# Performance work log

Hardware: AMD Instinct MI355X
Metric: run time of the kernel (lower is better)

The kernel has to match this reference:

```python
import jax, jax.numpy as jnp
import numpy as np

B, T, C, H, RANK = 4, 2048, 1024, 16, 8


def _lora_linear(x, W, b, A, Bm):
    # loralib-style: y = x W^T + b + (x A^T) B^T  (scaling alpha/r = 1)
    return x @ W.T + b + (x @ A.T) @ Bm.T


def setup_inputs() -> dict:
    key = jax.random.key(0)
    ks = jax.random.split(key, 6)
    s_in = 1.0 / np.sqrt(C)
    return {
        "x": jax.random.normal(ks[0], (B, T, C), jnp.float32),
        "c_attn_w": jax.random.normal(ks[1], (3 * C, C), jnp.float32) * s_in,
        "c_attn_b": jnp.zeros((3 * C,), jnp.float32),
        "c_attn_A": jax.random.normal(ks[2], (RANK, C), jnp.float32) * s_in,
        "c_attn_B": jnp.zeros((3 * C, RANK), jnp.float32),
        "c_proj_w": jax.random.normal(ks[3], (C, C), jnp.float32) * s_in,
        "c_proj_b": jnp.zeros((C,), jnp.float32),
        "c_proj_A": jax.random.normal(ks[4], (RANK, C), jnp.float32) * s_in,
        "c_proj_B": jnp.zeros((C, RANK), jnp.float32),
        "n_head": H,
    }


def reference(x, c_attn_w, c_attn_b, c_attn_A, c_attn_B,
              c_proj_w, c_proj_b, c_proj_A, c_proj_B, n_head):
    Bsz, Tlen, Cd = x.shape
    d = Cd // n_head
    qkv = _lora_linear(x, c_attn_w, c_attn_b, c_attn_A, c_attn_B)  # [B,T,3C]
    q, k, v = jnp.split(qkv, 3, axis=2)
    query, key_out = q, k  # returned pre-reshape, as in torch
    # [B, H, T, d]
    qh = q.reshape(Bsz, Tlen, n_head, d).transpose(0, 2, 1, 3)
    kh = k.reshape(Bsz, Tlen, n_head, d).transpose(0, 2, 1, 3)
    vh = v.reshape(Bsz, Tlen, n_head, d).transpose(0, 2, 1, 3)
    att = jnp.einsum('bhqd,bhkd->bhqk', qh, kh) * (1.0 / np.sqrt(d))
    causal = jnp.tril(jnp.ones((Tlen, Tlen), bool))
    att = jnp.where(causal[None, None], att, -jnp.inf)
    att = jax.nn.softmax(att, axis=-1)
    y = jnp.einsum('bhqk,bhkd->bhqd', att, vh)
    y = y.transpose(0, 2, 1, 3).reshape(Bsz, Tlen, Cd)
    out = _lora_linear(y, c_proj_w, c_proj_b, c_proj_A, c_proj_B)
    return out, query, key_out
```

## Files before the change

### kernel.cpp

```cpp
#include <hip/hip_runtime.h>
#include <stdint.h>

#define T_LEN 2048
#define C_DIM 1024
#define NHEAD 16
#define DHEAD 64
#define QOFF  8388608L
#define KOFF  16777216L
#define SCALE_LOG2 0.18033688011112042f

typedef float f32x4 __attribute__((ext_vector_type(4)));
typedef short bf16x8 __attribute__((ext_vector_type(8)));
typedef short s16x4 __attribute__((ext_vector_type(4)));
typedef unsigned short u16;

__device__ __forceinline__ float b2f(u16 h) {
  union { uint32_t u; float f; } v; v.u = ((uint32_t)h) << 16; return v.f;
}
__device__ __forceinline__ u16 f2b(float f) {
  union { float f; uint32_t u; } v; v.f = f;
  uint32_t r = v.u + 0x7fffu + ((v.u >> 16) & 1u);
  return (u16)(r >> 16);
}
__device__ __forceinline__ u16 f2b_tr(float f) {
  union { float f; uint32_t u; } v; v.f = f;
  return (u16)(v.u >> 16);
}
__device__ __forceinline__ void async16(const u16* g, u16* l) {
  __builtin_amdgcn_global_load_lds((const __attribute__((address_space(1))) void*)g,
                                   (__attribute__((address_space(3))) void*)l, 16, 0, 0);
}

#define MFMA16 __builtin_amdgcn_mfma_f32_16x16x32_bf16

__global__ __launch_bounds__(256) void prep_all(const float* __restrict__ x,
                                                u16* __restrict__ xc,
                                                const float* __restrict__ w1,
                                                const float* __restrict__ B1,
                                                const float* __restrict__ A1,
                                                u16* __restrict__ w1e,
                                                const float* __restrict__ w2,
                                                const float* __restrict__ B2,
                                                const float* __restrict__ A2,
                                                u16* __restrict__ w2e) {
  int b = blockIdx.x;
  if (b < 8192) {
    long i = ((long)b * 256 + threadIdx.x) * 4;
    f32x4 v = *(const f32x4*)(x + i);
    s16x4 r;
    r[0] = (short)f2b(v[0]); r[1] = (short)f2b(v[1]);
    r[2] = (short)f2b(v[2]); r[3] = (short)f2b(v[3]);
    *(s16x4*)(xc + i) = r;
  } else if (b < 20480) {
    int i = (b - 8192) * 256 + threadIdx.x;
    int n = i >> 10, k = i & 1023;
    float acc = w1[i];
#pragma unroll
    for (int r = 0; r < 8; r++) acc += B1[n * 8 + r] * A1[r * 1024 + k];
    w1e[i] = f2b(acc);
  } else {
    int i = (b - 20480) * 256 + threadIdx.x;
    int n = i >> 10, k = i & 1023;
    float acc = w2[i];
#pragma unroll
    for (int r = 0; r < 8; r++) acc += B2[n * 8 + r] * A2[r * 1024 + k];
    w2e[i] = f2b(acc);
  }
}

template <int MODE>
__global__ __launch_bounds__(256) void gemm_bt(const u16* __restrict__ A,
                                               const u16* __restrict__ Bt,
                                               const float* __restrict__ bias,
                                               float* __restrict__ outf,
                                               u16* __restrict__ kc,
                                               u16* __restrict__ vblk, int K) {
  __shared__ __align__(16) u16 ldsA[128 * 32];
  __shared__ __align__(16) u16 ldsB[128 * 32];
  const int t = threadIdx.x;
  const int lane = t & 63, l15 = lane & 15, quad = lane >> 4, w = t >> 6;
  const int wr = (w >> 1) * 64, wc = (w & 1) * 64;
  const long rowA = (long)blockIdx.y * 128;
  const long rowB = (long)blockIdx.x * 128;
  const int srow = t >> 2, scol = (t & 3) * 8;

  f32x4 acc[4][4];
#pragma unroll
  for (int i = 0; i < 4; i++)
#pragma unroll
    for (int j = 0; j < 4; j++) { f32x4 z = {0.f, 0.f, 0.f, 0.f}; acc[i][j] = z; }

  const u16* Ab = A + rowA * K;
  const u16* Bb = Bt + rowB * K;
  for (int k0 = 0; k0 < K; k0 += 32) {
    __syncthreads();
    async16(Ab + (long)srow * K + k0 + scol, &ldsA[t * 8]);
    async16(Ab + (long)(srow + 64) * K + k0 + scol, &ldsA[2048 + t * 8]);
    async16(Bb + (long)srow * K + k0 + scol, &ldsB[t * 8]);
    async16(Bb + (long)(srow + 64) * K + k0 + scol, &ldsB[2048 + t * 8]);
    __syncthreads();
    bf16x8 af[4], bfr[4];
#pragma unroll
    for (int g = 0; g < 4; g++) {
      af[g]  = *(const bf16x8*)&ldsA[(wr + g * 16 + l15) * 32 + quad * 8];
      bfr[g] = *(const bf16x8*)&ldsB[(wc + g * 16 + l15) * 32 + quad * 8];
    }
#pragma unroll
    for (int i = 0; i < 4; i++)
#pragma unroll
      for (int j = 0; j < 4; j++)
        acc[i][j] = MFMA16(af[i], bfr[j], acc[i][j], 0, 0, 0);
  }

#pragma unroll
  for (int i = 0; i < 4; i++) {
#pragma unroll
    for (int j = 0; j < 4; j++) {
      int n = (int)rowB + wc + j * 16 + l15;
      float bv = bias[n];
#pragma unroll
      for (int r = 0; r < 4; r++) {
        int m = (int)rowA + wr + i * 16 + quad * 4 + r;
        float val = acc[i][j][r] + bv;
        if constexpr (MODE == 1) {
          outf[(long)m * C_DIM + n] = val;
        } else {
          int sec = n >> 10;
          int nc = n & 1023;
          int h = nc >> 6, dd = nc & 63;
          int bb = m >> 11, tt = m & 2047;
          int bh = bb * NHEAD + h;
          if (sec == 0) {
            outf[QOFF + (long)m * C_DIM + nc] = val;
          } else if (sec == 1) {
            outf[KOFF + (long)m * C_DIM + nc] = val;
            kc[(long)bh * (T_LEN * 64) + (long)tt * 64 + dd] = f2b(val);
          } else {
            vblk[(long)bh * (T_LEN * 64) + (long)(tt >> 6) * 4096 + dd * 64 + (tt & 63)] = f2b(val);
          }
        }
      }
    }
  }
}

__global__ __launch_bounds__(256) void flash_attn(const float* __restrict__ qsec,
                                                  const u16* __restrict__ kc,
                                                  const u16* __restrict__ vblk,
                                                  u16* __restrict__ yb) {
  __shared__ __align__(16) u16 ldsK[2][64 * 64];
  __shared__ __align__(16) u16 ldsV[2][64 * 64];
  __shared__ __align__(16) u16 plds[4][32 * 72];
  const int t = threadIdx.x;
  const int lane = t & 63, l15 = lane & 15, quad = lane >> 4, w = t >> 6;
  const int p = blockIdx.x >> 6;
  const int bh = blockIdx.x & 63;
  const int bb = bh >> 4, h = bh & 15;

  bf16x8 ones;
#pragma unroll
  for (int j = 0; j < 8; j++) ones[j] = (short)0x3F80;

  const u16* kcb = kc + (long)bh * (T_LEN * 64);
  const u16* vbb = vblk + (long)bh * (T_LEN * 64);
  const int l0 = t, l1 = 256 + t;
  const int s0c = ((l0 >> 3) * 8 + ((l0 & 7) ^ ((l0 >> 3) & 7))) * 8;
  const int s1c = ((l1 >> 3) * 8 + ((l1 & 7) ^ ((l1 >> 3) & 7))) * 8;

#define KV_STAGE(kt_, b_) do {                                        \
    const u16* ks_ = kcb + (long)(kt_) * 4096;                        \
    const u16* vs_ = vbb + (long)(kt_) * 4096;                        \
    async16(ks_ + s0c, &ldsK[b_][l0 * 8]);                            \
    async16(ks_ + s1c, &ldsK[b_][l1 * 8]);                            \
    async16(vs_ + s0c, &ldsV[b_][l0 * 8]);                            \
    async16(vs_ + s1c, &ldsV[b_][l1 * 8]);                            \
  } while (0)

#pragma unroll 1
  for (int half = 0; half < 2; half++) {
    const int qt = half ? p : (15 - p);
    const int q0 = qt * 128;

    const float* Qb = qsec + ((long)bb * T_LEN + q0 + w * 32) * C_DIM + h * DHEAD;
    bf16x8 qf[2][2];
#pragma unroll
    for (int rg = 0; rg < 2; rg++)
#pragma unroll
      for (int kk = 0; kk < 2; kk++) {
        const float* ptr = Qb + (long)(rg * 16 + l15) * C_DIM + kk * 32 + quad * 8;
        f32x4 a = *(const f32x4*)ptr, b = *(const f32x4*)(ptr + 4);
        bf16x8 r;
        r[0] = (short)f2b(a[0] * SCALE_LOG2); r[1] = (short)f2b(a[1] * SCALE_LOG2);
        r[2] = (short)f2b(a[2] * SCALE_LOG2); r[3] = (short)f2b(a[3] * SCALE_LOG2);
        r[4] = (short)f2b(b[0] * SCALE_LOG2); r[5] = (short)f2b(b[1] * SCALE_LOG2);
        r[6] = (short)f2b(b[2] * SCALE_LOG2); r[7] = (short)f2b(b[3] * SCALE_LOG2);
        qf[rg][kk] = r;
      }

    f32x4 o[2][4];
    f32x4 ls[2];
#pragma unroll
    for (int rg = 0; rg < 2; rg++) {
#pragma unroll
      for (int cg = 0; cg < 4; cg++) { f32x4 z = {0.f, 0.f, 0.f, 0.f}; o[rg][cg] = z; }
      f32x4 z = {0.f, 0.f, 0.f, 0.f}; ls[rg] = z;
    }

    const int qminw = q0 + w * 32;
    const int nkt = (q0 + 128) >> 6;

    KV_STAGE(0, 0);
    asm volatile("s_waitcnt vmcnt(0)" ::: "memory");
    __builtin_amdgcn_s_barrier();

    for (int kt = 0; kt < nkt; kt++) {
      const int kb0 = kt * 64;
      const int cur = kt & 1;
      if (kt + 1 < nkt) KV_STAGE(kt + 1, cur ^ 1);

      if (kb0 <= qminw + 31) {
        f32x4 s[2][4];
#pragma unroll
        for (int rg = 0; rg < 2; rg++)
#pragma unroll
          for (int kg = 0; kg < 4; kg++) { f32x4 z = {0.f, 0.f, 0.f, 0.f}; s[rg][kg] = z; }
#pragma unroll
        for (int kg = 0; kg < 4; kg++) {
          int row = kg * 16 + l15, sw = row & 7;
          bf16x8 kf0 = *(const bf16x8*)&ldsK[cur][row * 64 + ((quad ^ sw) * 8)];
          bf16x8 kf1 = *(const bf16x8*)&ldsK[cur][row * 64 + (((4 + quad) ^ sw) * 8)];
#pragma unroll
          for (int rg = 0; rg < 2; rg++) {
            s[rg][kg] = MFMA16(qf[rg][0], kf0, s[rg][kg], 0, 0, 0);
            s[rg][kg] = MFMA16(qf[rg][1], kf1, s[rg][kg], 0, 0, 0);
          }
        }
        const bool needMask = (kb0 + 63) > qminw;
#pragma unroll
        for (int rg = 0; rg < 2; rg++) {
#pragma unroll
          for (int r = 0; r < 4; r++) {
            float v0 = s[rg][0][r], v1 = s[rg][1][r], v2 = s[rg][2][r], v3 = s[rg][3][r];
            if (needMask) {
              int qrow = qminw + rg * 16 + quad * 4 + r;
              if (kb0 + l15 > qrow)      v0 = -3.0e38f;
              if (kb0 + 16 + l15 > qrow) v1 = -3.0e38f;
              if (kb0 + 32 + l15 > qrow) v2 = -3.0e38f;
              if (kb0 + 48 + l15 > qrow) v3 = -3.0e38f;
            }
            int prow = rg * 16 + quad * 4 + r;
            plds[w][prow * 72 + l15]      = f2b_tr(exp2f(v0));
            plds[w][prow * 72 + 16 + l15] = f2b_tr(exp2f(v1));
            plds[w][prow * 72 + 32 + l15] = f2b_tr(exp2f(v2));
            plds[w][prow * 72 + 48 + l15] = f2b_tr(exp2f(v3));
          }
        }
        asm volatile("s_waitcnt lgkmcnt(0)" ::: "memory");
        bf16x8 pf[2][2];
#pragma unroll
        for (int rg = 0; rg < 2; rg++)
#pragma unroll
          for (int kk = 0; kk < 2; kk++)
            pf[rg][kk] = *(const bf16x8*)&plds[w][(rg * 16 + l15) * 72 + kk * 32 + quad * 8];
#pragma unroll
        for (int rg = 0; rg < 2; rg++) {
          ls[rg] = MFMA16(pf[rg][0], ones, ls[rg], 0, 0, 0);
          ls[rg] = MFMA16(pf[rg][1], ones, ls[rg], 0, 0, 0);
        }
#pragma unroll
        for (int cg = 0; cg < 4; cg++) {
          int row = cg * 16 + l15, sw = row & 7;
          bf16x8 vf0 = *(const bf16x8*)&ldsV[cur][row * 64 + ((quad ^ sw) * 8)];
          bf16x8 vf1 = *(const bf16x8*)&ldsV[cur][row * 64 + (((4 + quad) ^ sw) * 8)];
#pragma unroll
          for (int rg = 0; rg < 2; rg++) {
            o[rg][cg] = MFMA16(pf[rg][0], vf0, o[rg][cg], 0, 0, 0);
            o[rg][cg] = MFMA16(pf[rg][1], vf1, o[rg][cg], 0, 0, 0);
          }
        }
      }

      asm volatile("s_waitcnt vmcnt(0)" ::: "memory");
      __builtin_amdgcn_s_barrier();
    }

#pragma unroll
    for (int rg = 0; rg < 2; rg++) {
#pragma unroll
      for (int r = 0; r < 4; r++) {
        float inv = 1.0f / ls[rg][r];
        int tt = q0 + w * 32 + rg * 16 + quad * 4 + r;
        long base = ((long)bb * T_LEN + tt) * C_DIM + h * DHEAD;
#pragma unroll
        for (int cg = 0; cg < 4; cg++)
          yb[base + cg * 16 + l15] = f2b(o[rg][cg][r] * inv);
      }
    }
  }
}

extern "C" void kernel_launch(void* const* d_in, const int* in_sizes, int n_in,
                              void* d_out, int out_size, void* d_ws, size_t ws_size,
                              hipStream_t stream) {
  const float* x  = (const float*)d_in[0];
  const float* w1 = (const float*)d_in[1];
  const float* b1 = (const float*)d_in[2];
  const float* A1 = (const float*)d_in[3];
  const float* B1 = (const float*)d_in[4];
  const float* w2 = (const float*)d_in[5];
  const float* b2 = (const float*)d_in[6];
  const float* A2 = (const float*)d_in[7];
  const float* B2 = (const float*)d_in[8];
  float* outf = (float*)d_out;
  u16* outb16 = (u16*)d_out;

  u16* ws  = (u16*)d_ws;
  u16* w2e = ws;
  u16* w1e = ws + 1048576;
  u16* xc  = ws + 4194304;
  u16* yb  = ws + 1048576;
  u16* vblk = outb16;
  u16* kcp  = outb16 + 8388608;

  prep_all<<<24576, 256, 0, stream>>>(x, xc, w1, B1, A1, w1e, w2, B2, A2, w2e);
  gemm_bt<0><<<dim3(24, 64), 256, 0, stream>>>(xc, w1e, b1, outf, kcp, vblk, 1024);
  flash_attn<<<512, 256, 0, stream>>>(outf + QOFF, kcp, vblk, yb);
  gemm_bt<1><<<dim3(8, 64), 256, 0, stream>>>(yb, w2e, b2, outf, nullptr, nullptr, 1024);
}
```

Before: 355.8 us.

## Load K/V fragments directly from global memory and drop LDS staging

The flash attention kernel no longer stages K and V tiles into double-buffered shared memory with async copies and block barriers. Each wave now reads its K and V MFMA fragments straight from global memory and runs its own causal trip count. The launch also changes from 512 blocks that each processed a paired short and long query tile to 1024 blocks of one query tile each. This removes barrier sync and LDS footprint, which may allow higher occupancy. The cost is redundant global/L2 reads across the four waves, no explicit prefetch to hide load latency, and loss of the paired-tile load balancing.

Result: slower. 413.4 us (+16.2%).

```diff
diff --git a/kernel.cpp b/kernel.cpp
--- a/kernel.cpp
+++ b/kernel.cpp
@@ -148,153 +148,128 @@
                                                   const u16* __restrict__ kc,
                                                   const u16* __restrict__ vblk,
                                                   u16* __restrict__ yb) {
-  __shared__ __align__(16) u16 ldsK[2][64 * 64];
-  __shared__ __align__(16) u16 ldsV[2][64 * 64];
   __shared__ __align__(16) u16 plds[4][32 * 72];
   const int t = threadIdx.x;
   const int lane = t & 63, l15 = lane & 15, quad = lane >> 4, w = t >> 6;
-  const int p = blockIdx.x >> 6;
+  const int qt = 15 - (blockIdx.x >> 6);
   const int bh = blockIdx.x & 63;
+  const int q0 = qt * 128;
   const int bb = bh >> 4, h = bh & 15;
 
+  const float* Qb = qsec + ((long)bb * T_LEN + q0 + w * 32) * C_DIM + h * DHEAD;
+  bf16x8 qf[2][2];
+#pragma unroll
+  for (int rg = 0; rg < 2; rg++)
+#pragma unroll
+    for (int kk = 0; kk < 2; kk++) {
+      const float* p = Qb + (long)(rg * 16 + l15) * C_DIM + kk * 32 + quad * 8;
+      f32x4 a = *(const f32x4*)p, b = *(const f32x4*)(p + 4);
+      bf16x8 r;
+      r[0] = (short)f2b(a[0] * SCALE_LOG2); r[1] = (short)f2b(a[1] * SCALE_LOG2);
+      r[2] = (short)f2b(a[2] * SCALE_LOG2); r[3] = (short)f2b(a[3] * SCALE_LOG2);
+      r[4] = (short)f2b(b[0] * SCALE_LOG2); r[5] = (short)f2b(b[1] * SCALE_LOG2);
+      r[6] = (short)f2b(b[2] * SCALE_LOG2); r[7] = (short)f2b(b[3] * SCALE_LOG2);
+      qf[rg][kk] = r;
+    }
+
   bf16x8 ones;
 #pragma unroll
   for (int j = 0; j < 8; j++) ones[j] = (short)0x3F80;
+
+  f32x4 o[2][4];
+  f32x4 ls[2];
+#pragma unroll
+  for (int rg = 0; rg < 2; rg++) {
+#pragma unroll
+    for (int cg = 0; cg < 4; cg++) { f32x4 z = {0.f, 0.f, 0.f, 0.f}; o[rg][cg] = z; }
+    f32x4 z = {0.f, 0.f, 0.f, 0.f}; ls[rg] = z;
+  }
 
   const u16* kcb = kc + (long)bh * (T_LEN * 64);
   const u16* vbb = vblk + (long)bh * (T_LEN * 64);
-  const int l0 = t, l1 = 256 + t;
-  const int s0c = ((l0 >> 3) * 8 + ((l0 & 7) ^ ((l0 >> 3) & 7))) * 8;
-  const int s1c = ((l1 >> 3) * 8 + ((l1 & 7) ^ ((l1 >> 3) & 7))) * 8;
-
-#define KV_STAGE(kt_, b_) do {                                        \
-    const u16* ks_ = kcb + (long)(kt_) * 4096;                        \
-    const u16* vs_ = vbb + (long)(kt_) * 4096;                        \
-    async16(ks_ + s0c, &ldsK[b_][l0 * 8]);                            \
-    async16(ks_ + s1c, &ldsK[b_][l1 * 8]);                            \
-    async16(vs_ + s0c, &ldsV[b_][l0 * 8]);                            \
-    async16(vs_ + s1c, &ldsV[b_][l1 * 8]);                            \
-  } while (0)
-
-#pragma unroll 1
-  for (int half = 0; half < 2; half++) {
-    const int qt = half ? p : (15 - p);
-    const int q0 = qt * 128;
-
-    const float* Qb = qsec + ((long)bb * T_LEN + q0 + w * 32) * C_DIM + h * DHEAD;
-    bf16x8 qf[2][2];
+
+  const int qminw = q0 + w * 32;
+  const int nktw = (qminw + 95) >> 6;
+
+  for (int kt = 0; kt < nktw; kt++) {
+    const int kb0 = kt * 64;
+    const u16* ktb = kcb + (long)kb0 * 64;
+    const u16* vtb = vbb + (long)kt * 4096;
+
+    f32x4 s[2][4];
 #pragma unroll
     for (int rg = 0; rg < 2; rg++)
 #pragma unroll
-      for (int kk = 0; kk < 2; kk++) {
-        const float* ptr = Qb + (long)(rg * 16 + l15) * C_DIM + kk * 32 + quad * 8;
-        f32x4 a = *(const f32x4*)ptr, b = *(const f32x4*)(ptr + 4);
-        bf16x8 r;
-        r[0] = (short)f2b(a[0] * SCALE_LOG2); r[1] = (short)f2b(a[1] * SCALE_LOG2);
-        r[2] = (short)f2b(a[2] * SCALE_LOG2); r[3] = (short)f2b(a[3] * SCALE_LOG2);
-        r[4] = (short)f2b(b[0] * SCALE_LOG2); r[5] = (short)f2b(b[1] * SCALE_LOG2);
-        r[6] = (short)f2b(b[2] * SCALE_LOG2); r[7] = (short)f2b(b[3] * SCALE_LOG2);
-        qf[rg][kk] = r;
+      for (int kg = 0; kg < 4; kg++) { f32x4 z = {0.f, 0.f, 0.f, 0.f}; s[rg][kg] = z; }
+#pragma unroll
+    for (int kg = 0; kg < 4; kg++) {
+      int row = kg * 16 + l15;
+      bf16x8 kf0 = *(const bf16x8*)(ktb + row * 64 + quad * 8);
+      bf16x8 kf1 = *(const bf16x8*)(ktb + row * 64 + 32 + quad * 8);
+#pragma unroll
+      for (int rg = 0; rg < 2; rg++) {
+        s[rg][kg] = MFMA16(qf[rg][0], kf0, s[rg][kg], 0, 0, 0);
+        s[rg][kg] = MFMA16(qf[rg][1], kf1, s[rg][kg], 0, 0, 0);
       }
-
-    f32x4 o[2][4];
-    f32x4 ls[2];
+    }
+    const bool needMask = (kb0 + 63) > qminw;
 #pragma unroll
     for (int rg = 0; rg < 2; rg++) {
 #pragma unroll
-      for (int cg = 0; cg < 4; cg++) { f32x4 z = {0.f, 0.f, 0.f, 0.f}; o[rg][cg] = z; }
-      f32x4 z = {0.f, 0.f, 0.f, 0.f}; ls[rg] = z;
-    }
-
-    const int qminw = q0 + w * 32;
-    const int nkt = (q0 + 128) >> 6;
-
-    KV_STAGE(0, 0);
-    asm volatile("s_waitcnt vmcnt(0)" ::: "memory");
-    __builtin_amdgcn_s_barrier();
-
-    for (int kt = 0; kt < nkt; kt++) {
-      const int kb0 = kt * 64;
-      const int cur = kt & 1;
-      if (kt + 1 < nkt) KV_STAGE(kt + 1, cur ^ 1);
-
-      if (kb0 <= qminw + 31) {
-        f32x4 s[2][4];
-#pragma unroll
-        for (int rg = 0; rg < 2; rg++)
-#pragma unroll
-          for (int kg = 0; kg < 4; kg++) { f32x4 z = {0.f, 0.f, 0.f, 0.f}; s[rg][kg] = z; }
-#pragma unroll
-        for (int kg = 0; kg < 4; kg++) {
-          int row = kg * 16 + l15, sw = row & 7;
-          bf16x8 kf0 = *(const bf16x8*)&ldsK[cur][row * 64 + ((quad ^ sw) * 8)];
-          bf16x8 kf1 = *(const bf16x8*)&ldsK[cur][row * 64 + (((4 + quad) ^ sw) * 8)];
-#pragma unroll
-          for (int rg = 0; rg < 2; rg++) {
-            s[rg][kg] = MFMA16(qf[rg][0], kf0, s[rg][kg], 0, 0, 0);
-            s[rg][kg] = MFMA16(qf[rg][1], kf1, s[rg][kg], 0, 0, 0);
-          }
+      for (int r = 0; r < 4; r++) {
+        float v0 = s[rg][0][r], v1 = s[rg][1][r], v2 = s[rg][2][r], v3 = s[rg][3][r];
+        if (needMask) {
+          int qrow = qminw + rg * 16 + quad * 4 + r;
+          if (kb0 + l15 > qrow)      v0 = -3.0e38f;
+          if (kb0 + 16 + l15 > qrow) v1 = -3.0e38f;
+          if (kb0 + 32 + l15 > qrow) v2 = -3.0e38f;
+          if (kb0 + 48 + l15 > qrow) v3 = -3.0e38f;
         }
-        const bool needMask = (kb0 + 63) > qminw;
-#pragma unroll
-        for (int rg = 0; rg < 2; rg++) {
-#pragma unroll
-          for (int r = 0; r < 4; r++) {
-            float v0 = s[rg][0][r], v1 = s[rg][1][r], v2 = s[rg][2][r], v3 = s[rg][3][r];
-            if (needMask) {
-              int qrow = qminw + rg * 16 + quad * 4 + r;
-              if (kb0 + l15 > qrow)      v0 = -3.0e38f;
-              if (kb0 + 16 + l15 > qrow) v1 = -3.0e38f;
-              if (kb0 + 32 + l15 > qrow) v2 = -3.0e38f;
-              if (kb0 + 48 + l15 > qrow) v3 = -3.0e38f;
-            }
-            int prow = rg * 16 + quad * 4 + r;
-            plds[w][prow * 72 + l15]      = f2b_tr(exp2f(v0));
-            plds[w][prow * 72 + 16 + l15] = f2b_tr(exp2f(v1));
-            plds[w][prow * 72 + 32 + l15] = f2b_tr(exp2f(v2));
-            plds[w][prow * 72 + 48 + l15] = f2b_tr(exp2f(v3));
-          }
-        }
-        asm volatile("s_waitcnt lgkmcnt(0)" ::: "memory");
-        bf16x8 pf[2][2];
-#pragma unroll
-        for (int rg = 0; rg < 2; rg++)
-#pragma unroll
-          for (int kk = 0; kk < 2; kk++)
-            pf[rg][kk] = *(const bf16x8*)&plds[w][(rg * 16 + l15) * 72 + kk * 32 + quad * 8];
-#pragma unroll
-        for (int rg = 0; rg < 2; rg++) {
-          ls[rg] = MFMA16(pf[rg][0], ones, ls[rg], 0, 0, 0);
-          ls[rg] = MFMA16(pf[rg][1], ones, ls[rg], 0, 0, 0);
-        }
-#pragma unroll
-        for (int cg = 0; cg < 4; cg++) {
-          int row = cg * 16 + l15, sw = row & 7;
-          bf16x8 vf0 = *(const bf16x8*)&ldsV[cur][row * 64 + ((quad ^ sw) * 8)];
-          bf16x8 vf1 = *(const bf16x8*)&ldsV[cur][row * 64 + (((4 + quad) ^ sw) * 8)];
-#pragma unroll
-          for (int rg = 0; rg < 2; rg++) {
-            o[rg][cg] = MFMA16(pf[rg][0], vf0, o[rg][cg], 0, 0, 0);
-            o[rg][cg] = MFMA16(pf[rg][1], vf1, o[rg][cg], 0, 0, 0);
-          }
-        }
+        int prow = rg * 16 + quad * 4 + r;
+        plds[w][prow * 72 + l15]      = f2b_tr(exp2f(v0));
+        plds[w][prow * 72 + 16 + l15] = f2b_tr(exp2f(v1));
+        plds[w][prow * 72 + 32 + l15] = f2b_tr(exp2f(v2));
+        plds[w][prow * 72 + 48 + l15] = f2b_tr(exp2f(v3));
       }
-
-      asm volatile("s_waitcnt vmcnt(0)" ::: "memory");
-      __builtin_amdgcn_s_barrier();
-    }
-
+    }
+    bf16x8 vf[4][2];
+#pragma unroll
+    for (int cg = 0; cg < 4; cg++) {
+      int row = cg * 16 + l15;
+      vf[cg][0] = *(const bf16x8*)(vtb + row * 64 + quad * 8);
+      vf[cg][1] = *(const bf16x8*)(vtb + row * 64 + 32 + quad * 8);
+    }
+    asm volatile("s_waitcnt lgkmcnt(0)" ::: "memory");
+    bf16x8 pf[2][2];
+#pragma unroll
+    for (int rg = 0; rg < 2; rg++)
+#pragma unroll
+      for (int kk = 0; kk < 2; kk++)
+        pf[rg][kk] = *(const bf16x8*)&plds[w][(rg * 16 + l15) * 72 + kk * 32 + quad * 8];
 #pragma unroll
     for (int rg = 0; rg < 2; rg++) {
-#pragma unroll
-      for (int r = 0; r < 4; r++) {
-        float inv = 1.0f / ls[rg][r];
-        int tt = q0 + w * 32 + rg * 16 + quad * 4 + r;
-        long base = ((long)bb * T_LEN + tt) * C_DIM + h * DHEAD;
-#pragma unroll
-        for (int cg = 0; cg < 4; cg++)
-          yb[base + cg * 16 + l15] = f2b(o[rg][cg][r] * inv);
+      ls[rg] = MFMA16(pf[rg][0], ones, ls[rg], 0, 0, 0);
+      ls[rg] = MFMA16(pf[rg][1], ones, ls[rg], 0, 0, 0);
+    }
+#pragma unroll
+    for (int cg = 0; cg < 4; cg++) {
+#pragma unroll
+      for (int rg = 0; rg < 2; rg++) {
+        o[rg][cg] = MFMA16(pf[rg][0], vf[cg][0], o[rg][cg], 0, 0, 0);
+        o[rg][cg] = MFMA16(pf[rg][1], vf[cg][1], o[rg][cg], 0, 0, 0);
       }
+    }
+  }
+#pragma unroll
+  for (int rg = 0; rg < 2; rg++) {
+#pragma unroll
+    for (int r = 0; r < 4; r++) {
+      float inv = 1.0f / ls[rg][r];
+      int tt = q0 + w * 32 + rg * 16 + quad * 4 + r;
+      long base = ((long)bb * T_LEN + tt) * C_DIM + h * DHEAD;
+#pragma unroll
+      for (int cg = 0; cg < 4; cg++)
+        yb[base + cg * 16 + l15] = f2b(o[rg][cg][r] * inv);
     }
   }
 }
@@ -324,6 +299,6 @@
 
   prep_all<<<24576, 256, 0, stream>>>(x, xc, w1, B1, A1, w1e, w2, B2, A2, w2e);
   gemm_bt<0><<<dim3(24, 64), 256, 0, stream>>>(xc, w1e, b1, outf, kcp, vblk, 1024);
-  flash_attn<<<512, 256, 0, stream>>>(outf + QOFF, kcp, vblk, yb);
+  flash_attn<<<1024, 256, 0, stream>>>(outf + QOFF, kcp, vblk, yb);
   gemm_bt<1><<<dim3(8, 64), 256, 0, stream>>>(yb, w2e, b2, outf, nullptr, nullptr, 1024);
 }
```
